# Performance work log

Hardware: AMD Instinct MI355X
Metric: run time of the kernel (lower is better)

Reference implementation:

```python
import jax, jax.numpy as jnp
import numpy as np

N, D, E = 16384, 1024, 8

def setup_inputs() -> dict:
    key = jax.random.key(0)
    ks = jax.random.split(key, 5)
    s = 1.0 / np.sqrt(D)
    return {
        "x": jax.random.normal(ks[0], (N, D), dtype=jnp.float32),
        "router_w": jax.random.uniform(ks[1], (E, D), jnp.float32, -s, s),   # torch Linear weight [out,in]
        "router_b": jax.random.uniform(ks[2], (E,), jnp.float32, -s, s),
        "expert_w": jax.random.uniform(ks[3], (E, D, D), jnp.float32, -s, s),  # [E, out, in]
        "expert_b": jax.random.uniform(ks[4], (E, D), jnp.float32, -s, s),
    }

def reference(x, router_w, router_b, expert_w, expert_b):
    # Router: logits -> softmax -> argmax (argmax of softmax == argmax of logits)
    logits = x @ router_w.T + router_b            # [N, E]
    top = jnp.argmax(logits, axis=-1)             # [N]
    # Compute all expert outputs (vectorized grouped GEMM), then select top-1.
    # Faithful to the torch loop: output is the raw expert output, NOT gate-scaled.
    xe = jnp.einsum('nd,eod->neo', x, expert_w) + expert_b[None, :, :]  # [N, E, D]
    out = jnp.take_along_axis(xe, top[:, None, None], axis=1)[:, 0, :]  # [N, D]
    return out
```

## Files before the change

kernel.cpp:

```cpp
#include <hip/hip_runtime.h>
#include <hip/hip_bf16.h>


#define NTOK 16384
#define DIM  1024
#define NEXP 8

typedef __bf16 bf16x8 __attribute__((ext_vector_type(8)));
typedef float  f32x4  __attribute__((ext_vector_type(4)));

__device__ __forceinline__ unsigned int f2bf(float f) {
  unsigned int u = __builtin_bit_cast(unsigned int, f);
  u += 0x7FFFu + ((u >> 16) & 1u);
  return u >> 16;
}

__global__ __launch_bounds__(256) void k_convw(const float* __restrict__ src,
                                               unsigned short* __restrict__ dst) {
  size_t i = ((size_t)blockIdx.x * 256 + threadIdx.x) * 8;
  const float4* p = (const float4*)(src + i);
  float4 a = p[0], b = p[1];
  unsigned int w0 = f2bf(a.x) | (f2bf(a.y) << 16);
  unsigned int w1 = f2bf(a.z) | (f2bf(a.w) << 16);
  unsigned int w2 = f2bf(b.x) | (f2bf(b.y) << 16);
  unsigned int w3 = f2bf(b.z) | (f2bf(b.w) << 16);
  *(uint4*)(dst + i) = make_uint4(w0, w1, w2, w3);
}

__global__ __launch_bounds__(256) void k_router(const float* __restrict__ x,
                                                const float* __restrict__ rw,
                                                const float* __restrict__ rb,
                                                unsigned short* __restrict__ xbf,
                                                int* __restrict__ top) {
  __shared__ float wlds[NEXP * DIM];
  const int tid = threadIdx.x;
  const int lane = tid & 63;
  const int wave = tid >> 6;
#pragma unroll
  for (int i = 0; i < 8; ++i)
    ((float4*)wlds)[tid + 256 * i] = ((const float4*)rw)[tid + 256 * i];
  __syncthreads();

  const int ea = lane & 7;
  const float bias = rb[ea];

#pragma unroll 1
  for (int tp = 0; tp < 2; ++tp) {
    const int nA = (blockIdx.x << 4) + (wave << 2) + (tp << 1);
    const int nB = nA + 1;

    float4 xa[4], xb[4];
#pragma unroll
    for (int j = 0; j < 4; ++j) {
      xa[j] = *(const float4*)(x + ((size_t)nA << 10) + (j << 8) + (lane << 2));
      xb[j] = *(const float4*)(x + ((size_t)nB << 10) + (j << 8) + (lane << 2));
    }

#pragma unroll
    for (int j = 0; j < 4; ++j) {
      uint2 sa, sb;
      sa.x = f2bf(xa[j].x) | (f2bf(xa[j].y) << 16);
      sa.y = f2bf(xa[j].z) | (f2bf(xa[j].w) << 16);
      sb.x = f2bf(xb[j].x) | (f2bf(xb[j].y) << 16);
      sb.y = f2bf(xb[j].z) | (f2bf(xb[j].w) << 16);
      *(uint2*)(xbf + ((size_t)nA << 10) + (j << 8) + (lane << 2)) = sa;
      *(uint2*)(xbf + ((size_t)nB << 10) + (j << 8) + (lane << 2)) = sb;
    }

    double pA[8] = {}, pB[8] = {};
#pragma unroll
    for (int j = 0; j < 4; ++j) {
#pragma unroll
      for (int e = 0; e < 8; ++e) {
        float4 wv = *(const float4*)&wlds[e * 1024 + (j << 8) + (lane << 2)];
        pA[e] += (double)xa[j].x * (double)wv.x;
        pA[e] += (double)xa[j].y * (double)wv.y;
        pA[e] += (double)xa[j].z * (double)wv.z;
        pA[e] += (double)xa[j].w * (double)wv.w;
        pB[e] += (double)xb[j].x * (double)wv.x;
        pB[e] += (double)xb[j].y * (double)wv.y;
        pB[e] += (double)xb[j].z * (double)wv.z;
        pB[e] += (double)xb[j].w * (double)wv.w;
      }
      __builtin_amdgcn_sched_barrier(0);
    }

    float qA[8], qB[8];
#pragma unroll
    for (int e = 0; e < 8; ++e) { qA[e] = (float)pA[e]; qB[e] = (float)pB[e]; }
#pragma unroll
    for (int e = 0; e < 8; ++e) {
      qA[e] += __shfl_xor(qA[e], 1);
      qB[e] += __shfl_xor(qB[e], 1);
      qA[e] += __shfl_xor(qA[e], 2);
      qB[e] += __shfl_xor(qB[e], 2);
      qA[e] += __shfl_xor(qA[e], 4);
      qB[e] += __shfl_xor(qB[e], 4);
    }
    float sA, sB;
    {
      float q0 = (ea & 1) ? qA[1] : qA[0], q1 = (ea & 1) ? qA[3] : qA[2];
      float q2 = (ea & 1) ? qA[5] : qA[4], q3 = (ea & 1) ? qA[7] : qA[6];
      float r0 = (ea & 2) ? q1 : q0, r1 = (ea & 2) ? q3 : q2;
      sA = (ea & 4) ? r1 : r0;
      q0 = (ea & 1) ? qB[1] : qB[0]; q1 = (ea & 1) ? qB[3] : qB[2];
      q2 = (ea & 1) ? qB[5] : qB[4]; q3 = (ea & 1) ? qB[7] : qB[6];
      r0 = (ea & 2) ? q1 : q0; r1 = (ea & 2) ? q3 : q2;
      sB = (ea & 4) ? r1 : r0;
    }
    sA += __shfl_xor(sA, 8);  sB += __shfl_xor(sB, 8);
    sA += __shfl_xor(sA, 16); sB += __shfl_xor(sB, 16);
    sA += __shfl_xor(sA, 32); sB += __shfl_xor(sB, 32);
    sA += bias; sB += bias;
    float bvA = sA, bvB = sB;
    int biA = ea, biB = ea;
#pragma unroll
    for (int mask = 1; mask <= 4; mask <<= 1) {
      float ovA = __shfl_xor(bvA, mask), ovB = __shfl_xor(bvB, mask);
      int oiA = __shfl_xor(biA, mask), oiB = __shfl_xor(biB, mask);
      if (ovA > bvA || (ovA == bvA && oiA < biA)) { bvA = ovA; biA = oiA; }
      if (ovB > bvB || (ovB == bvB && oiB < biB)) { bvB = ovB; biB = oiB; }
    }
    if (lane == 0) {
      top[nA] = biA;
      top[nB] = biB;
    }
  }
}

__global__ __launch_bounds__(1024) void k_sort(const int* __restrict__ top,
                                               int* __restrict__ counts,
                                               int* __restrict__ tok) {
  __shared__ unsigned long long sc[2][2][1024];
  const int t = threadIdx.x;

  int4 v[4];
  const int4* tp = (const int4*)(top + t * 16);
#pragma unroll
  for (int i = 0; i < 4; ++i) v[i] = tp[i];

  unsigned long long h0 = 0, h1 = 0;
#pragma unroll
  for (int i = 0; i < 16; ++i) {
    int e = ((const int*)v)[i];
    if (e < 4) h0 += 1ull << (16 * e);
    else       h1 += 1ull << (16 * (e - 4));
  }
  sc[0][0][t] = h0;
  sc[0][1][t] = h1;
  __syncthreads();

  int cur = 0;
  for (int s = 1; s < 1024; s <<= 1) {
    unsigned long long a0 = sc[cur][0][t], a1 = sc[cur][1][t];
    if (t >= s) { a0 += sc[cur][0][t - s]; a1 += sc[cur][1][t - s]; }
    sc[cur ^ 1][0][t] = a0;
    sc[cur ^ 1][1][t] = a1;
    cur ^= 1;
    __syncthreads();
  }

  unsigned long long b0 = sc[cur][0][t] - h0;
  unsigned long long b1 = sc[cur][1][t] - h1;
  if (t == 1023) {
    unsigned long long i0 = sc[cur][0][t], i1 = sc[cur][1][t];
#pragma unroll
    for (int e = 0; e < 4; ++e) counts[e] = (int)((i0 >> (16 * e)) & 0xFFFF);
#pragma unroll
    for (int e = 0; e < 4; ++e) counts[4 + e] = (int)((i1 >> (16 * e)) & 0xFFFF);
  }
#pragma unroll
  for (int i = 0; i < 16; ++i) {
    int e = ((const int*)v)[i];
    int pos;
    if (e < 4) {
      pos = (int)((b0 >> (16 * e)) & 0xFFFF);
      b0 += 1ull << (16 * e);
    } else {
      int f = e - 4;
      pos = (int)((b1 >> (16 * f)) & 0xFFFF);
      b1 += 1ull << (16 * f);
    }
    tok[(e << 14) + pos] = t * 16 + i;
  }
}

__global__ __launch_bounds__(256) void k_gemm(const unsigned short* __restrict__ xbf,
                                              const unsigned short* __restrict__ wbf,
                                              const float* __restrict__ eb,
                                              const int* __restrict__ counts,
                                              const int* __restrict__ tokall,
                                              float* __restrict__ out) {
  const int bid = blockIdx.x;
  const int e = bid & 7;
  const int loc = bid >> 3;
  const int cb = loc & 7;
  const int t = loc >> 3;
  const int c = counts[e];
  if (t * 128 >= c) return;
  const int n0 = cb << 7;
  const int* tok = tokall + (e << 14);
  const int tid = threadIdx.x;
  const int lane = tid & 63;
  const int wave = tid >> 6;

  __shared__ unsigned short As[2][128 * 32];
  __shared__ unsigned short Bs[2][128 * 32];

  const int prow = tid >> 2;
  const int pchk = tid & 3;
  size_t asrc[2], bsrc[2];
  const unsigned short* wb = wbf + ((size_t)e << 20);
#pragma unroll
  for (int s = 0; s < 2; ++s) {
    int row = s * 64 + prow;
    int m = t * 128 + row;
    int g = tok[(m < c) ? m : 0];
    int l = pchk ^ ((row ^ (row >> 2)) & 3);
    asrc[s] = (size_t)g * DIM + (size_t)l * 8;
    bsrc[s] = (size_t)(n0 + row) * DIM + (size_t)l * 8;
  }

  f32x4 acc[4][4] = {};
  const int wr = wave >> 1, wc = wave & 1;

  int aoff[4], boff[4];
#pragma unroll
  for (int m = 0; m < 4; ++m) {
    int row = wr * 64 + m * 16 + (lane & 15);
    int p = ((lane >> 4) ^ (row ^ (row >> 2))) & 3;
    aoff[m] = row * 32 + p * 8;
    int rowb = wc * 64 + m * 16 + (lane & 15);
    int pb = ((lane >> 4) ^ (rowb ^ (rowb >> 2))) & 3;
    boff[m] = rowb * 32 + pb * 8;
  }

  auto stage = [&](int b, int k0) {
#pragma unroll
    for (int s = 0; s < 2; ++s) {
      __builtin_amdgcn_global_load_lds(
          (const __attribute__((address_space(1))) unsigned int*)(xbf + asrc[s] + k0),
          (__attribute__((address_space(3))) unsigned int*)(&As[b][s * 2048 + wave * 512]),
          16, 0, 0);
      __builtin_amdgcn_global_load_lds(
          (const __attribute__((address_space(1))) unsigned int*)(wb + bsrc[s] + k0),
          (__attribute__((address_space(3))) unsigned int*)(&Bs[b][s * 2048 + wave * 512]),
          16, 0, 0);
    }
  };

  stage(0, 0);
  for (int k = 0; k < 32; ++k) {
    if (k < 31) {
      stage((k + 1) & 1, (k + 1) * 32);
      asm volatile("s_waitcnt vmcnt(4)" ::: "memory");
    } else {
      asm volatile("s_waitcnt vmcnt(0)" ::: "memory");
    }
    __builtin_amdgcn_s_barrier();
    __builtin_amdgcn_sched_barrier(0);
    const unsigned short* Ab = As[k & 1];
    const unsigned short* Bb = Bs[k & 1];
    bf16x8 af[4], bfr[4];
#pragma unroll
    for (int m = 0; m < 4; ++m) af[m] = *(const bf16x8*)&Ab[aoff[m]];
#pragma unroll
    for (int n = 0; n < 4; ++n) bfr[n] = *(const bf16x8*)&Bb[boff[n]];
#pragma unroll
    for (int m = 0; m < 4; ++m)
#pragma unroll
      for (int n = 0; n < 4; ++n)
        acc[m][n] = __builtin_amdgcn_mfma_f32_16x16x32_bf16(af[m], bfr[n], acc[m][n], 0, 0, 0);
    __builtin_amdgcn_s_barrier();
  }

  const int colb = n0 + wc * 64 + (lane & 15);
  float bias[4];
#pragma unroll
  for (int n = 0; n < 4; ++n) bias[n] = eb[(e << 10) + colb + n * 16];
#pragma unroll
  for (int m = 0; m < 4; ++m) {
    int rbase = t * 128 + wr * 64 + m * 16 + ((lane >> 4) << 2);
#pragma unroll
    for (int r = 0; r < 4; ++r) {
      int mm = rbase + r;
      if (mm < c) {
        int g = tok[mm];
        float* op = out + ((size_t)g << 10);
#pragma unroll
        for (int n = 0; n < 4; ++n) op[colb + n * 16] = acc[m][n][r] + bias[n];
      }
    }
  }
}

extern "C" void kernel_launch(void* const* d_in, const int* in_sizes, int n_in,
                              void* d_out, int out_size, void* d_ws, size_t ws_size,
                              hipStream_t stream) {
  const float* x  = (const float*)d_in[0];
  const float* rw = (const float*)d_in[1];
  const float* rb = (const float*)d_in[2];
  const float* ew = (const float*)d_in[3];
  const float* eb = (const float*)d_in[4];
  float* out = (float*)d_out;

  char* ws = (char*)d_ws;
  unsigned short* wbf = (unsigned short*)ws;
  unsigned short* xbf = (unsigned short*)(ws + (16u << 20));
  int* tok    = (int*)(ws + (48u << 20));
  int* counts = (int*)(ws + (48u << 20) + (1u << 19));
  int* top    = (int*)(ws + (48u << 20) + (1u << 19) + 128);

  k_convw<<<4096, 256, 0, stream>>>(ew, wbf);
  k_router<<<NTOK / 16, 256, 0, stream>>>(x, rw, rb, xbf, top);
  k_sort<<<1, 1024, 0, stream>>>(top, counts, tok);
  k_gemm<<<8192, 256, 0, stream>>>(xbf, wbf, eb, counts, tok, out);
}
```

Baseline: 113.5 us.

## Enlarge grouped GEMM tiles to 256x256x64 with 8 waves and interleaved prefetch

```diff
diff --git a/kernel.cpp b/kernel.cpp
--- a/kernel.cpp
+++ b/kernel.cpp
@@ -5,6 +5,9 @@
 #define NTOK 16384
 #define DIM  1024
 #define NEXP 8
+
+#define AS1 __attribute__((address_space(1)))
+#define AS3 __attribute__((address_space(3)))
 
 typedef __bf16 bf16x8 __attribute__((ext_vector_type(8)));
 typedef float  f32x4  __attribute__((ext_vector_type(4)));
@@ -185,102 +188,162 @@
   }
 }
 
-__global__ __launch_bounds__(256) void k_gemm(const unsigned short* __restrict__ xbf,
-                                              const unsigned short* __restrict__ wbf,
-                                              const float* __restrict__ eb,
-                                              const int* __restrict__ counts,
-                                              const int* __restrict__ tokall,
-                                              float* __restrict__ out) {
+__global__ __launch_bounds__(512, 2) void k_gemm(const unsigned short* __restrict__ xbf,
+                                                 const unsigned short* __restrict__ wbf,
+                                                 const float* __restrict__ eb,
+                                                 const int* __restrict__ counts,
+                                                 const int* __restrict__ tokall,
+                                                 float* __restrict__ out) {
   const int bid = blockIdx.x;
   const int e = bid & 7;
   const int loc = bid >> 3;
-  const int cb = loc & 7;
-  const int t = loc >> 3;
+  const int nt = loc & 3;
+  const int mt = loc >> 2;
   const int c = counts[e];
-  if (t * 128 >= c) return;
-  const int n0 = cb << 7;
-  const int* tok = tokall + (e << 14);
+  if (mt * 256 >= c) return;
   const int tid = threadIdx.x;
   const int lane = tid & 63;
-  const int wave = tid >> 6;
-
-  __shared__ unsigned short As[2][128 * 32];
-  __shared__ unsigned short Bs[2][128 * 32];
-
-  const int prow = tid >> 2;
-  const int pchk = tid & 3;
-  size_t asrc[2], bsrc[2];
+  const int w = tid >> 6;
+  const int wr = w >> 2;
+  const int wn = w & 3;
+  const int* tok = tokall + (e << 14);
   const unsigned short* wb = wbf + ((size_t)e << 20);
-#pragma unroll
-  for (int s = 0; s < 2; ++s) {
-    int row = s * 64 + prow;
-    int m = t * 128 + row;
-    int g = tok[(m < c) ? m : 0];
-    int l = pchk ^ ((row ^ (row >> 2)) & 3);
-    asrc[s] = (size_t)g * DIM + (size_t)l * 8;
-    bsrc[s] = (size_t)(n0 + row) * DIM + (size_t)l * 8;
-  }
-
-  f32x4 acc[4][4] = {};
-  const int wr = wave >> 1, wc = wave & 1;
-
-  int aoff[4], boff[4];
-#pragma unroll
-  for (int m = 0; m < 4; ++m) {
-    int row = wr * 64 + m * 16 + (lane & 15);
-    int p = ((lane >> 4) ^ (row ^ (row >> 2))) & 3;
-    aoff[m] = row * 32 + p * 8;
-    int rowb = wc * 64 + m * 16 + (lane & 15);
-    int pb = ((lane >> 4) ^ (rowb ^ (rowb >> 2))) & 3;
-    boff[m] = rowb * 32 + pb * 8;
-  }
-
-  auto stage = [&](int b, int k0) {
+
+  __shared__ unsigned short As[2][256 * 64];
+  __shared__ unsigned short Bs[2][256 * 64];
+
+  unsigned abase[2][2], bbase[2][2];
+#pragma unroll
+  for (int hf = 0; hf < 2; ++hf)
 #pragma unroll
     for (int s = 0; s < 2; ++s) {
+      int ci = s * 512 + tid;
+      int row = hf * 128 + (ci >> 3);
+      int l = (ci & 7) ^ (row & 7);
+      int m = mt * 256 + row;
+      int g = tok[(m < c) ? m : 0];
+      abase[hf][s] = (unsigned)(g * DIM + l * 8);
+      bbase[hf][s] = (unsigned)((nt * 256 + row) * DIM + l * 8);
+    }
+  const unsigned ldst = (unsigned)((w << 6) << 3);
+
+  unsigned aoff[2][8], boff[2][4];
+#pragma unroll
+  for (int kh = 0; kh < 2; ++kh) {
+#pragma unroll
+    for (int i = 0; i < 8; ++i) {
+      int r = wr * 128 + i * 16 + (lane & 15);
+      int p = ((kh << 2) + (lane >> 4)) ^ (r & 7);
+      aoff[kh][i] = r * 64 + p * 8;
+    }
+#pragma unroll
+    for (int j = 0; j < 4; ++j) {
+      int r = wn * 64 + j * 16 + (lane & 15);
+      int p = ((kh << 2) + (lane >> 4)) ^ (r & 7);
+      boff[kh][j] = r * 64 + p * 8;
+    }
+  }
+
+  auto stage = [&](int buf, int mat, int hf, int k0) {
+    unsigned short* lds = mat ? &Bs[buf][0] : &As[buf][0];
+    const unsigned short* src = mat ? wb : xbf;
+    const unsigned* base = mat ? bbase[hf] : abase[hf];
+#pragma unroll
+    for (int s = 0; s < 2; ++s)
       __builtin_amdgcn_global_load_lds(
-          (const __attribute__((address_space(1))) unsigned int*)(xbf + asrc[s] + k0),
-          (__attribute__((address_space(3))) unsigned int*)(&As[b][s * 2048 + wave * 512]),
+          (const AS1 unsigned int*)(src + base[s] + k0),
+          (AS3 unsigned int*)(lds + hf * 8192 + s * 4096 + ldst),
           16, 0, 0);
-      __builtin_amdgcn_global_load_lds(
-          (const __attribute__((address_space(1))) unsigned int*)(wb + bsrc[s] + k0),
-          (__attribute__((address_space(3))) unsigned int*)(&Bs[b][s * 2048 + wave * 512]),
-          16, 0, 0);
-    }
   };
 
-  stage(0, 0);
-  for (int k = 0; k < 32; ++k) {
-    if (k < 31) {
-      stage((k + 1) & 1, (k + 1) * 32);
-      asm volatile("s_waitcnt vmcnt(4)" ::: "memory");
-    } else {
-      asm volatile("s_waitcnt vmcnt(0)" ::: "memory");
-    }
-    __builtin_amdgcn_s_barrier();
+  stage(0, 0, 0, 0); stage(0, 0, 1, 0); stage(0, 1, 0, 0); stage(0, 1, 1, 0);
+  asm volatile("s_waitcnt vmcnt(0)" ::: "memory");
+  __builtin_amdgcn_s_barrier();
+
+  f32x4 acc[8][4] = {};
+  bf16x8 af[4], bf[4];
+
+#pragma unroll 1
+  for (int kt = 0; kt < 16; ++kt) {
+    const int buf = kt & 1;
+    const int k0n = (kt + 1) << 6;
+    const unsigned short* Ab = &As[buf][0];
+    const unsigned short* Bb = &Bs[buf][0];
+    const bool pre = kt < 15;
+
+#pragma unroll
+    for (int j = 0; j < 4; ++j) bf[j] = *(const bf16x8*)&Bb[boff[0][j]];
+#pragma unroll
+    for (int i = 0; i < 4; ++i) af[i] = *(const bf16x8*)&Ab[aoff[0][i]];
+    if (pre) stage(buf ^ 1, 0, 0, k0n);
+    __builtin_amdgcn_s_barrier();
+    asm volatile("s_waitcnt lgkmcnt(0)" ::: "memory");
     __builtin_amdgcn_sched_barrier(0);
-    const unsigned short* Ab = As[k & 1];
-    const unsigned short* Bb = Bs[k & 1];
-    bf16x8 af[4], bfr[4];
-#pragma unroll
-    for (int m = 0; m < 4; ++m) af[m] = *(const bf16x8*)&Ab[aoff[m]];
-#pragma unroll
-    for (int n = 0; n < 4; ++n) bfr[n] = *(const bf16x8*)&Bb[boff[n]];
-#pragma unroll
-    for (int m = 0; m < 4; ++m)
-#pragma unroll
-      for (int n = 0; n < 4; ++n)
-        acc[m][n] = __builtin_amdgcn_mfma_f32_16x16x32_bf16(af[m], bfr[n], acc[m][n], 0, 0, 0);
-    __builtin_amdgcn_s_barrier();
-  }
-
-  const int colb = n0 + wc * 64 + (lane & 15);
+    __builtin_amdgcn_s_setprio(1);
+#pragma unroll
+    for (int i = 0; i < 4; ++i)
+#pragma unroll
+      for (int j = 0; j < 4; ++j)
+        acc[i][j] = __builtin_amdgcn_mfma_f32_16x16x32_bf16(af[i], bf[j], acc[i][j], 0, 0, 0);
+    __builtin_amdgcn_s_setprio(0);
+    __builtin_amdgcn_s_barrier();
+
+#pragma unroll
+    for (int i = 0; i < 4; ++i) af[i] = *(const bf16x8*)&Ab[aoff[0][4 + i]];
+    if (pre) stage(buf ^ 1, 0, 1, k0n);
+    __builtin_amdgcn_s_barrier();
+    asm volatile("s_waitcnt lgkmcnt(0)" ::: "memory");
+    __builtin_amdgcn_sched_barrier(0);
+    __builtin_amdgcn_s_setprio(1);
+#pragma unroll
+    for (int i = 0; i < 4; ++i)
+#pragma unroll
+      for (int j = 0; j < 4; ++j)
+        acc[4 + i][j] = __builtin_amdgcn_mfma_f32_16x16x32_bf16(af[i], bf[j], acc[4 + i][j], 0, 0, 0);
+    __builtin_amdgcn_s_setprio(0);
+    __builtin_amdgcn_s_barrier();
+
+#pragma unroll
+    for (int j = 0; j < 4; ++j) bf[j] = *(const bf16x8*)&Bb[boff[1][j]];
+#pragma unroll
+    for (int i = 0; i < 4; ++i) af[i] = *(const bf16x8*)&Ab[aoff[1][i]];
+    if (pre) stage(buf ^ 1, 1, 0, k0n);
+    __builtin_amdgcn_s_barrier();
+    asm volatile("s_waitcnt lgkmcnt(0)" ::: "memory");
+    __builtin_amdgcn_sched_barrier(0);
+    __builtin_amdgcn_s_setprio(1);
+#pragma unroll
+    for (int i = 0; i < 4; ++i)
+#pragma unroll
+      for (int j = 0; j < 4; ++j)
+        acc[i][j] = __builtin_amdgcn_mfma_f32_16x16x32_bf16(af[i], bf[j], acc[i][j], 0, 0, 0);
+    __builtin_amdgcn_s_setprio(0);
+    __builtin_amdgcn_s_barrier();
+
+#pragma unroll
+    for (int i = 0; i < 4; ++i) af[i] = *(const bf16x8*)&Ab[aoff[1][4 + i]];
+    if (pre) stage(buf ^ 1, 1, 1, k0n);
+    __builtin_amdgcn_s_barrier();
+    asm volatile("s_waitcnt lgkmcnt(0)" ::: "memory");
+    __builtin_amdgcn_sched_barrier(0);
+    __builtin_amdgcn_s_setprio(1);
+#pragma unroll
+    for (int i = 0; i < 4; ++i)
+#pragma unroll
+      for (int j = 0; j < 4; ++j)
+        acc[4 + i][j] = __builtin_amdgcn_mfma_f32_16x16x32_bf16(af[i], bf[j], acc[4 + i][j], 0, 0, 0);
+    __builtin_amdgcn_s_setprio(0);
+    asm volatile("s_waitcnt vmcnt(0)" ::: "memory");
+    __builtin_amdgcn_s_barrier();
+  }
+
+  const int colb = (nt << 8) + (wn << 6) + (lane & 15);
   float bias[4];
 #pragma unroll
-  for (int n = 0; n < 4; ++n) bias[n] = eb[(e << 10) + colb + n * 16];
-#pragma unroll
-  for (int m = 0; m < 4; ++m) {
-    int rbase = t * 128 + wr * 64 + m * 16 + ((lane >> 4) << 2);
+  for (int j = 0; j < 4; ++j) bias[j] = eb[(e << 10) + colb + j * 16];
+#pragma unroll
+  for (int i = 0; i < 8; ++i) {
+    int rbase = (mt << 8) + (wr << 7) + i * 16 + ((lane >> 4) << 2);
 #pragma unroll
     for (int r = 0; r < 4; ++r) {
       int mm = rbase + r;
@@ -288,7 +351,7 @@
         int g = tok[mm];
         float* op = out + ((size_t)g << 10);
 #pragma unroll
-        for (int n = 0; n < 4; ++n) op[colb + n * 16] = acc[m][n][r] + bias[n];
+        for (int j = 0; j < 4; ++j) op[colb + j * 16] = acc[i][j][r] + bias[j];
       }
     }
   }
@@ -314,5 +377,5 @@
   k_convw<<<4096, 256, 0, stream>>>(ew, wbf);
   k_router<<<NTOK / 16, 256, 0, stream>>>(x, rw, rb, xbf, top);
   k_sort<<<1, 1024, 0, stream>>>(top, counts, tok);
-  k_gemm<<<8192, 256, 0, stream>>>(xbf, wbf, eb, counts, tok, out);
-}
+  k_gemm<<<2048, 512, 0, stream>>>(xbf, wbf, eb, counts, tok, out);
+}
```

Result: slower. 119.5 us (+5.3%).
